# Kernel optimization log

Measured on AMD Instinct MI355X. Metric: run time of the kernel, lower is better.

Reference implementation:

```python
import jax, jax.numpy as jnp
import numpy as np

N, M, D, O = 1_000_000, 64, 3, 2


def _rbf(A, B, sf, ell):
    # squared-exponential kernel: sf^2 * exp(-||a/ell - b/ell||^2 / 2)
    A = A / ell
    B = B / ell
    sq = (jnp.sum(A * A, axis=1)[:, None]
          + jnp.sum(B * B, axis=1)[None, :]
          - 2.0 * (A @ B.T))
    return (sf * sf) * jnp.exp(-sq / 2.0)


def setup_inputs() -> dict:
    key = jax.random.key(0)
    k1, k2, k3, k4 = jax.random.split(key, 4)
    X = jax.random.uniform(k1, (N, D), dtype=jnp.float32) * 10.0  # query points
    t = jax.random.normal(k2, (N,), dtype=jnp.float32)            # unused by forward (matches torch)
    Z = jax.random.uniform(k3, (M, D), dtype=jnp.float32) * 10.0  # inducing points (well-separated -> Kzz well-conditioned)
    U = jax.random.normal(k4, (M, O), dtype=jnp.float32)          # learned inducing outputs
    return {"t": t, "X": X, "Z": Z, "U": U, "sf": 1.0, "ell": 1.0}


def reference(t, X, Z, U, sf, ell):
    # Precompute (as in __init__): Kzz, its inverse, Cholesky factor, and their product.
    Kzz = _rbf(Z, Z, sf, ell)                      # [M, M]
    L = jnp.linalg.cholesky(Kzz)                   # [M, M]
    KzzinvL = jnp.linalg.inv(Kzz) @ L              # [M, M]
    # Forward: T = K(X, Z) @ KzzinvL ; out = T @ U
    Kxz = _rbf(X, Z, sf, ell)                      # [N, M] -- dominant memory traffic
    return (Kxz @ KzzinvL) @ U                     # [N, O]
```

## Files before the change

kernel.cpp:

```cpp
#include <hip/hip_runtime.h>
#include <hip/hip_bf16.h>
#include <utility>

#define LOG2E 1.4426950408889634f

#if __has_builtin(__builtin_amdgcn_exp2f)
#define EXP2F(x) __builtin_amdgcn_exp2f(x)
#else
#define EXP2F(x) exp2f(x)
#endif

#if __has_builtin(__builtin_amdgcn_rsqf)
#define RSQ(x) __builtin_amdgcn_rsqf(x)
#else
#define RSQ(x) (1.0f / sqrtf(x))
#endif

#define RDLANE(x, l) __int_as_float(__builtin_amdgcn_readlane(__float_as_int(x), (l)))

typedef float f16v __attribute__((ext_vector_type(16)));
struct Rows { f16v v0, v1, v2, v3; };

template<int J> __device__ __forceinline__ float getR(const Rows& r) {
    if constexpr (J < 16)      return r.v0[J];
    else if constexpr (J < 32) return r.v1[J - 16];
    else if constexpr (J < 48) return r.v2[J - 32];
    else                       return r.v3[J - 48];
}
template<int J> __device__ __forceinline__ void setR(Rows& r, float x) {
    if constexpr (J < 16)      r.v0[J] = x;
    else if constexpr (J < 32) r.v1[J - 16] = x;
    else if constexpr (J < 48) r.v2[J - 32] = x;
    else                       r.v3[J - 48] = x;
}

template<int LO, int W>
__device__ __forceinline__ float selR(const Rows& r, int k) {
    if constexpr (W == 1) {
        return getR<LO>(r);
    } else {
        float lo = selR<LO, W / 2>(r, k);
        float hi = selR<LO + W / 2, W / 2>(r, k);
        return (k & (W / 2)) ? hi : lo;
    }
}

template<int Q>
__device__ __forceinline__ void upd_quad(Rows& r, float lk, const float4 lv) {
    setR<4 * Q + 0>(r, fmaf(-lk, lv.x, getR<4 * Q + 0>(r)));
    setR<4 * Q + 1>(r, fmaf(-lk, lv.y, getR<4 * Q + 1>(r)));
    setR<4 * Q + 2>(r, fmaf(-lk, lv.z, getR<4 * Q + 2>(r)));
    setR<4 * Q + 3>(r, fmaf(-lk, lv.w, getR<4 * Q + 3>(r)));
}
template<int QLO, int... Qs>
__device__ __forceinline__ void upd_quads(Rows& r, float lk, const float4* lkb4,
                                          std::integer_sequence<int, Qs...>) {
    (upd_quad<QLO + Qs>(r, lk, lkb4[QLO + Qs]), ...);
}

template<int... Js>
__device__ __forceinline__ void load_row(Rows& r, const float* Lrow,
                                         std::integer_sequence<int, Js...>) {
    (setR<Js>(r, Lrow[Js]), ...);
}

template<int KLO, int KHI, int ULO>
__device__ __forceinline__ void chol_phase(Rows& r, float* Lsh, float* lkbuf,
                                           int lane) {
    const float4* lkb4 = (const float4*)lkbuf;
#pragma clang loop unroll(disable)
    for (int k = KLO; k < KHI; ++k) {
        float rk  = selR<ULO, 64 - ULO>(r, k);
        float dk  = RDLANE(rk, k);
        float inv = RSQ(dk);
        float lk  = rk * inv;
        float st  = (lane == k) ? inv : lk;
        Lsh[lane * 65 + k] = st;
        lkbuf[lane] = lk;
        upd_quads<ULO / 4>(r, lk, lkb4,
                           std::make_integer_sequence<int, 16 - ULO / 4>{});
    }
}

__global__ __launch_bounds__(64, 1)
void gp_precompute(const float* __restrict__ Z, const float* __restrict__ U,
                   const float* __restrict__ sf_p, const float* __restrict__ ell_p,
                   float* __restrict__ ws) {
    __shared__ float Lsh[64 * 65];
    __shared__ float4 zbuf[64];
    __shared__ __align__(16) float lkbuf[64];
    const int lane = threadIdx.x;
    const float sf  = sf_p[0];
    const float ell = ell_p[0];
    const float inv_ell = 1.0f / ell;
    const float sf2 = sf * sf;

    const float z0 = Z[lane * 3 + 0] * inv_ell;
    const float z1 = Z[lane * 3 + 1] * inv_ell;
    const float z2 = Z[lane * 3 + 2] * inv_ell;

    zbuf[lane] = make_float4(z0, z1, z2, 0.0f);
    __syncthreads();

#pragma unroll 4
    for (int j = 0; j < 64; ++j) {
        float4 zj = zbuf[j];
        float dx = z0 - zj.x;
        float dy = z1 - zj.y;
        float dz = z2 - zj.z;
        float sq = dx * dx + dy * dy + dz * dz;
        Lsh[lane * 65 + j] = sf2 * EXP2F(-0.5f * LOG2E * sq);
    }
    __syncthreads();

    Rows r;
    load_row(r, &Lsh[lane * 65], std::make_integer_sequence<int, 64>{});

    chol_phase< 0, 32,  0>(r, Lsh, lkbuf, lane);
    chol_phase<32, 48, 32>(r, Lsh, lkbuf, lane);
    chol_phase<48, 64, 48>(r, Lsh, lkbuf, lane);
    __syncthreads();

    float s0 = U[lane * 2 + 0];
    float s1 = U[lane * 2 + 1];
    float w0v = 0.0f, w1v = 0.0f;
#pragma unroll 8
    for (int i = 63; i >= 0; --i) {
        float a   = Lsh[i * 65 + lane];
        float rdi = RDLANE(a, i);
        float w0  = RDLANE(s0, i) * rdi;
        float w1  = RDLANE(s1, i) * rdi;
        bool  me  = (lane == i);
        w0v = me ? w0 : w0v;
        w1v = me ? w1 : w1v;
        s0 = fmaf(-a, w0, s0);
        s1 = fmaf(-a, w1, s1);
    }

    const float dm = -0.5f * LOG2E * (z0 * z0 + z1 * z1 + z2 * z2);
    float4* ws4 = (float4*)ws;
    ws4[lane * 2 + 0] = make_float4(z0, z1, z2, dm);
    ws4[lane * 2 + 1] = make_float4(sf2 * w0v, sf2 * w1v, 0.0f, 0.0f);
}

__global__ __launch_bounds__(256) void gp_forward(const float* __restrict__ X,
                                                  const float* __restrict__ ws,
                                                  const float* __restrict__ ell_p,
                                                  float* __restrict__ out,
                                                  int n, int nChunks) {
    __shared__ float4 P[128];
    for (int i = threadIdx.x; i < 128; i += 256)
        P[i] = ((const float4*)ws)[i];
    const float inv_ell = 1.0f / ell_p[0];
    __syncthreads();

    for (int chunk = blockIdx.x; chunk < nChunks; chunk += gridDim.x) {
        const int t  = chunk * 256 + (int)threadIdx.x;
        const int i0 = 2 * t;

        float p00, p01, p02, p10, p11, p12;
        if (i0 + 1 < n) {
            const float2* X2 = (const float2*)X;
            float2 xa = X2[3 * t + 0];
            float2 xb = X2[3 * t + 1];
            float2 xc = X2[3 * t + 2];
            p00 = xa.x; p01 = xa.y; p02 = xb.x;
            p10 = xb.y; p11 = xc.x; p12 = xc.y;
        } else if (i0 < n) {
            p00 = X[3 * i0 + 0]; p01 = X[3 * i0 + 1]; p02 = X[3 * i0 + 2];
            p10 = p00; p11 = p01; p12 = p02;
        } else {
            p00 = p01 = p02 = p10 = p11 = p12 = 0.0f;
        }

        float xt0[2], xt1[2], xt2[2], c[2];
        {
            float xs0 = p00 * inv_ell, xs1 = p01 * inv_ell, xs2 = p02 * inv_ell;
            c[0]  = -0.5f * LOG2E * (xs0 * xs0 + xs1 * xs1 + xs2 * xs2);
            xt0[0] = xs0 * LOG2E; xt1[0] = xs1 * LOG2E; xt2[0] = xs2 * LOG2E;
            xs0 = p10 * inv_ell; xs1 = p11 * inv_ell; xs2 = p12 * inv_ell;
            c[1]  = -0.5f * LOG2E * (xs0 * xs0 + xs1 * xs1 + xs2 * xs2);
            xt0[1] = xs0 * LOG2E; xt1[1] = xs1 * LOG2E; xt2[1] = xs2 * LOG2E;
        }

        float acc0[2] = {0.f, 0.f};
        float acc1[2] = {0.f, 0.f};

#pragma unroll 4
        for (int m = 0; m < 64; ++m) {
            const float4 a = P[2 * m + 0];
            const float4 b = P[2 * m + 1];
#pragma unroll
            for (int p = 0; p < 2; ++p) {
                float arg = fmaf(xt0[p], a.x,
                            fmaf(xt1[p], a.y,
                            fmaf(xt2[p], a.z, c[p] + a.w)));
                float e = EXP2F(arg);
                acc0[p] = fmaf(e, b.x, acc0[p]);
                acc1[p] = fmaf(e, b.y, acc1[p]);
            }
        }

        if (i0 + 1 < n) {
            ((float4*)out)[t] = make_float4(acc0[0], acc1[0], acc0[1], acc1[1]);
        } else if (i0 < n) {
            ((float2*)out)[i0] = make_float2(acc0[0], acc1[0]);
        }
    }
}

extern "C" void kernel_launch(void* const* d_in, const int* in_sizes, int n_in,
                              void* d_out, int out_size, void* d_ws, size_t ws_size,
                              hipStream_t stream) {
    const float* X    = (const float*)d_in[1];
    const float* Z    = (const float*)d_in[2];
    const float* U    = (const float*)d_in[3];
    const float* sf   = (const float*)d_in[4];
    const float* ell  = (const float*)d_in[5];
    float* out = (float*)d_out;
    float* ws  = (float*)d_ws;
    const int N = in_sizes[1] / 3;

    gp_precompute<<<1, 64, 0, stream>>>(Z, U, sf, ell, ws);

    const int nChunks = (N + 511) / 512;
    int blocks = (nChunks + 1) / 2;
    if (blocks < 1) blocks = 1;
    gp_forward<<<blocks, 256, 0, stream>>>(X, ws, ell, out, N, nChunks);
}
```

Baseline: 38.58 us.

## Block Cholesky in the precompute kernel into groups of four columns

Rewrites the single-wave Cholesky factorization to process four columns per iteration. A small 4x4 panel is factored with readlane broadcasts, then one rank-4 trailing update reads float4 entries from LDS. This cuts the number of serial loop iterations, LDS round trips and selR selections by a factor of four, aiming to shorten the latency-bound precompute. In exchange it adds more register pressure and longer dependent chains inside the panel.

```diff
diff --git a/kernel.cpp b/kernel.cpp
--- a/kernel.cpp
+++ b/kernel.cpp
@@ -45,40 +45,62 @@
     }
 }
 
-template<int Q>
-__device__ __forceinline__ void upd_quad(Rows& r, float lk, const float4 lv) {
-    setR<4 * Q + 0>(r, fmaf(-lk, lv.x, getR<4 * Q + 0>(r)));
-    setR<4 * Q + 1>(r, fmaf(-lk, lv.y, getR<4 * Q + 1>(r)));
-    setR<4 * Q + 2>(r, fmaf(-lk, lv.z, getR<4 * Q + 2>(r)));
-    setR<4 * Q + 3>(r, fmaf(-lk, lv.w, getR<4 * Q + 3>(r)));
-}
-template<int QLO, int... Qs>
-__device__ __forceinline__ void upd_quads(Rows& r, float lk, const float4* lkb4,
-                                          std::integer_sequence<int, Qs...>) {
-    (upd_quad<QLO + Qs>(r, lk, lkb4[QLO + Qs]), ...);
-}
-
 template<int... Js>
 __device__ __forceinline__ void load_row(Rows& r, const float* Lrow,
                                          std::integer_sequence<int, Js...>) {
     (setR<Js>(r, Lrow[Js]), ...);
 }
 
-template<int KLO, int KHI, int ULO>
-__device__ __forceinline__ void chol_phase(Rows& r, float* Lsh, float* lkbuf,
-                                           int lane) {
-    const float4* lkb4 = (const float4*)lkbuf;
+template<int Q>
+__device__ __forceinline__ void upd4(Rows& r, float lk0, float lk1, float lk2,
+                                     float lk3, const float4* lkb) {
+    float4 L0 = lkb[4 * Q + 0];
+    float4 L1 = lkb[4 * Q + 1];
+    float4 L2 = lkb[4 * Q + 2];
+    float4 L3 = lkb[4 * Q + 3];
+    setR<4*Q+0>(r, fmaf(-lk3, L0.w, fmaf(-lk2, L0.z, fmaf(-lk1, L0.y, fmaf(-lk0, L0.x, getR<4*Q+0>(r))))));
+    setR<4*Q+1>(r, fmaf(-lk3, L1.w, fmaf(-lk2, L1.z, fmaf(-lk1, L1.y, fmaf(-lk0, L1.x, getR<4*Q+1>(r))))));
+    setR<4*Q+2>(r, fmaf(-lk3, L2.w, fmaf(-lk2, L2.z, fmaf(-lk1, L2.y, fmaf(-lk0, L2.x, getR<4*Q+2>(r))))));
+    setR<4*Q+3>(r, fmaf(-lk3, L3.w, fmaf(-lk2, L3.z, fmaf(-lk1, L3.y, fmaf(-lk0, L3.x, getR<4*Q+3>(r))))));
+}
+template<int QLO, int... Qs>
+__device__ __forceinline__ void upd4_all(Rows& r, float lk0, float lk1,
+                                         float lk2, float lk3, const float4* lkb,
+                                         std::integer_sequence<int, Qs...>) {
+    (upd4<QLO + Qs>(r, lk0, lk1, lk2, lk3, lkb), ...);
+}
+
+template<int GLO, int GHI, int ULO>
+__device__ __forceinline__ void chol_groups(Rows& r, float* Lsh,
+                                            float4* lkbuf4, int lane) {
 #pragma clang loop unroll(disable)
-    for (int k = KLO; k < KHI; ++k) {
-        float rk  = selR<ULO, 64 - ULO>(r, k);
-        float dk  = RDLANE(rk, k);
-        float inv = RSQ(dk);
-        float lk  = rk * inv;
-        float st  = (lane == k) ? inv : lk;
-        Lsh[lane * 65 + k] = st;
-        lkbuf[lane] = lk;
-        upd_quads<ULO / 4>(r, lk, lkb4,
-                           std::make_integer_sequence<int, 16 - ULO / 4>{});
+    for (int g = GLO; g < GHI; ++g) {
+        const int k0 = 4 * g;
+        float t0 = selR<ULO, 64 - ULO>(r, k0 + 0);
+        float t1 = selR<ULO, 64 - ULO>(r, k0 + 1);
+        float t2 = selR<ULO, 64 - ULO>(r, k0 + 2);
+        float t3 = selR<ULO, 64 - ULO>(r, k0 + 3);
+        float i0  = RSQ(RDLANE(t0, k0 + 0));
+        float lk0 = t0 * i0;
+        t1 = fmaf(-lk0, RDLANE(lk0, k0 + 1), t1);
+        t2 = fmaf(-lk0, RDLANE(lk0, k0 + 2), t2);
+        t3 = fmaf(-lk0, RDLANE(lk0, k0 + 3), t3);
+        float i1  = RSQ(RDLANE(t1, k0 + 1));
+        float lk1 = t1 * i1;
+        t2 = fmaf(-lk1, RDLANE(lk1, k0 + 2), t2);
+        t3 = fmaf(-lk1, RDLANE(lk1, k0 + 3), t3);
+        float i2  = RSQ(RDLANE(t2, k0 + 2));
+        float lk2 = t2 * i2;
+        t3 = fmaf(-lk2, RDLANE(lk2, k0 + 3), t3);
+        float i3  = RSQ(RDLANE(t3, k0 + 3));
+        float lk3 = t3 * i3;
+        Lsh[lane * 65 + k0 + 0] = (lane == k0 + 0) ? i0 : lk0;
+        Lsh[lane * 65 + k0 + 1] = (lane == k0 + 1) ? i1 : lk1;
+        Lsh[lane * 65 + k0 + 2] = (lane == k0 + 2) ? i2 : lk2;
+        Lsh[lane * 65 + k0 + 3] = (lane == k0 + 3) ? i3 : lk3;
+        lkbuf4[lane] = make_float4(lk0, lk1, lk2, lk3);
+        upd4_all<ULO / 4>(r, lk0, lk1, lk2, lk3, lkbuf4,
+                          std::make_integer_sequence<int, 16 - ULO / 4>{});
     }
 }
 
@@ -88,7 +110,7 @@
                    float* __restrict__ ws) {
     __shared__ float Lsh[64 * 65];
     __shared__ float4 zbuf[64];
-    __shared__ __align__(16) float lkbuf[64];
+    __shared__ float4 lkbuf4[64];
     const int lane = threadIdx.x;
     const float sf  = sf_p[0];
     const float ell = ell_p[0];
@@ -116,9 +138,9 @@
     Rows r;
     load_row(r, &Lsh[lane * 65], std::make_integer_sequence<int, 64>{});
 
-    chol_phase< 0, 32,  0>(r, Lsh, lkbuf, lane);
-    chol_phase<32, 48, 32>(r, Lsh, lkbuf, lane);
-    chol_phase<48, 64, 48>(r, Lsh, lkbuf, lane);
+    chol_groups< 0,  8,  0>(r, Lsh, lkbuf4, lane);
+    chol_groups< 8, 12, 32>(r, Lsh, lkbuf4, lane);
+    chol_groups<12, 16, 48>(r, Lsh, lkbuf4, lane);
     __syncthreads();
 
     float s0 = U[lane * 2 + 0];
```

Measured after the change: 43.70 us. 13.3% more time.
